# Performance work log

Hardware: AMD Instinct MI355X
Metric: run time of the kernel (lower is better)

The kernel has to match this reference:

```python
import jax, jax.numpy as jnp
import numpy as np

NUM_HEADS = 16


def setup_inputs() -> dict:
    key = jax.random.key(0)
    k1, k2, k3 = jax.random.split(key, 3)
    B, S, E = 2, 2048, 1024
    hidden_states = jax.random.normal(k1, (B, S, E), dtype=jnp.float32)
    c_attn_w = jax.random.normal(k2, (E, 3 * E), dtype=jnp.float32) * 0.02
    c_attn_b = jnp.zeros((3 * E,), dtype=jnp.float32)
    c_proj_w = jax.random.normal(k3, (E, E), dtype=jnp.float32) * 0.02
    c_proj_b = jnp.zeros((E,), dtype=jnp.float32)
    return {
        "hidden_states": hidden_states,
        "c_attn_w": c_attn_w,
        "c_attn_b": c_attn_b,
        "c_proj_w": c_proj_w,
        "c_proj_b": c_proj_b,
    }


def reference(hidden_states, c_attn_w, c_attn_b, c_proj_w, c_proj_b):
    B, S, E = hidden_states.shape
    H = NUM_HEADS
    D = E // H
    # Conv1D: qkv projection -> [B, S, 3E]
    qkv = jnp.einsum("bse,ef->bsf", hidden_states, c_attn_w) + c_attn_b
    q, k, v = jnp.split(qkv, 3, axis=-1)
    # split heads -> [B, H, S, D]
    def heads(x):
        return x.reshape(B, S, H, D).transpose(0, 2, 1, 3)
    q, k, v = heads(q), heads(k), heads(v)
    # scaled QK^T -> [B, H, S, S]
    scale = jnp.asarray(D, dtype=q.dtype) ** 0.5
    attn_weights = jnp.einsum("bhqd,bhkd->bhqk", q, k) / scale
    # causal mask (bias buffer): True on/below diagonal
    causal = jnp.tril(jnp.ones((S, S), dtype=bool))
    mask_value = jnp.finfo(attn_weights.dtype).min
    attn_weights = jnp.where(causal[None, None, :, :], attn_weights, mask_value)
    attn_weights = jax.nn.softmax(attn_weights, axis=-1)
    # attn @ V -> merge heads -> [B, S, E]
    attn_out = jnp.einsum("bhqk,bhkd->bhqd", attn_weights, v)
    attn_out = attn_out.transpose(0, 2, 1, 3).reshape(B, S, E)
    # output projection (Conv1D)
    out = jnp.einsum("bse,ef->bsf", attn_out, c_proj_w) + c_proj_b
    return out
```

## Files before the change

kernel.cpp:

```cpp
#include <hip/hip_runtime.h>
#include <stdint.h>

typedef __attribute__((ext_vector_type(8))) __bf16 bf16x8;
typedef __attribute__((ext_vector_type(4))) __bf16 bf16x4;
typedef __attribute__((ext_vector_type(4))) float f32x4;

#define MFMA16(a, b, c) __builtin_amdgcn_mfma_f32_16x16x32_bf16(a, b, c, 0, 0, 0)

__device__ __forceinline__ void async_ld16(const __bf16* g, __bf16* lds_base) {
    __builtin_amdgcn_global_load_lds(
        (const __attribute__((address_space(1))) void*)g,
        (__attribute__((address_space(3))) void*)lds_base, 16, 0, 0);
}

__global__ __launch_bounds__(256) void k_prep(
    const float* __restrict__ hs, const float* __restrict__ w1,
    const float* __restrict__ w2, __bf16* __restrict__ hsb,
    __bf16* __restrict__ w1t, __bf16* __restrict__ w2t) {
    __shared__ __bf16 tile[32][33];
    int bid = blockIdx.x, tid = threadIdx.x;
    if (bid < 4096) {
        int i = (bid * 256 + tid) * 4;
        float4 v = *(const float4*)(hs + i);
        bf16x4 o;
        o.x = (__bf16)v.x; o.y = (__bf16)v.y; o.z = (__bf16)v.z; o.w = (__bf16)v.w;
        *(bf16x4*)(hsb + i) = o;
        return;
    }
    const float* in; __bf16* out; int C, tb;
    if (bid < 7168) { in = w1; out = w1t; C = 3072; tb = bid - 4096; }
    else            { in = w2; out = w2t; C = 1024; tb = bid - 7168; }
    const int R = 1024;
    int ntc = C >> 5;
    int c0 = (tb % ntc) * 32, r0 = (tb / ntc) * 32;
    int tx = tid & 31, ty = tid >> 5;
#pragma unroll
    for (int i = 0; i < 4; i++)
        tile[ty + i * 8][tx] = (__bf16)in[(size_t)(r0 + ty + i * 8) * C + c0 + tx];
    __syncthreads();
#pragma unroll
    for (int i = 0; i < 4; i++)
        out[(size_t)(c0 + ty + i * 8) * R + r0 + tx] = tile[tx][ty + i * 8];
}

__global__ __launch_bounds__(256, 3) void k_gemm_qkv(
    const __bf16* __restrict__ A, const __bf16* __restrict__ Bt,
    const float* __restrict__ bias,
    __bf16* __restrict__ Qo, __bf16* __restrict__ Ko, __bf16* __restrict__ Vo) {
    __shared__ __bf16 As[128 * 64];
    __shared__ __bf16 Bs[128 * 64];
    const int Kd = 1024;
    int lid = blockIdx.x;
    int xcd = lid & 7, c = lid >> 3;
    int mi = (xcd >> 1) * 8 + c / 12;
    int ni = (xcd & 1) * 12 + c % 12;
    int n0 = ni * 128, m0 = mi * 128;
    bool tr = (ni < 16);
    int tid = threadIdx.x;
    int wv = tid >> 6, lane = tid & 63;
    int wm = (wv >> 1) * 64, wn = (wv & 1) * 64;
    int quad = lane >> 4, l16 = lane & 15;
    int rl = lane >> 3, sj = lane & 7;
    int sgo = (sj ^ rl) << 3;
    int swl = l16 & 7;
    const __bf16* p0 = tr ? Bs : As;
    const __bf16* p1 = tr ? As : Bs;
    int o0 = tr ? wn : wm, o1 = tr ? wm : wn;
    f32x4 acc[4][4] = {};
    for (int k0 = 0; k0 < Kd; k0 += 64) {
        __syncthreads();
#pragma unroll
        for (int r = 0; r < 4; r++) {
            int row = wv * 32 + r * 8;
            async_ld16(&A[(size_t)(m0 + row + rl) * Kd + k0 + sgo], &As[row * 64]);
            async_ld16(&Bt[(size_t)(n0 + row + rl) * Kd + k0 + sgo], &Bs[row * 64]);
        }
        __syncthreads();
#pragma unroll
        for (int ks = 0; ks < 2; ks++) {
            bf16x8 f0[4], f1[4];
#pragma unroll
            for (int i = 0; i < 4; i++)
                f0[i] = *(const bf16x8*)(
                    &p0[(o0 + i * 16 + l16) * 64 + (((ks * 4 + quad) ^ swl) << 3)]);
#pragma unroll
            for (int j = 0; j < 4; j++)
                f1[j] = *(const bf16x8*)(
                    &p1[(o1 + j * 16 + l16) * 64 + (((ks * 4 + quad) ^ swl) << 3)]);
#pragma unroll
            for (int i = 0; i < 4; i++)
#pragma unroll
                for (int j = 0; j < 4; j++)
                    acc[i][j] = MFMA16(f0[i], f1[j], acc[i][j]);
        }
    }
    if (tr) {
#pragma unroll
        for (int i = 0; i < 4; i++) {
#pragma unroll
            for (int j = 0; j < 4; j++) {
                int nb = n0 + wn + i * 16 + quad * 4;
                int sec = nb >> 10, nl = nb & 1023;
                int h = nl >> 6, d = nl & 63;
                int sg = m0 + wm + j * 16 + l16;
                int bb = sg >> 11, s = sg & 2047;
                f32x4 bv = *(const f32x4*)(&bias[nb]);
                __bf16* dst = (sec == 0) ? Qo : Ko;
                float scl = (sec == 0) ? 0.1803368801f : 1.0f;
                bf16x4 q4;
#pragma unroll
                for (int r = 0; r < 4; r++)
                    q4[r] = (__bf16)((acc[i][j][r] + bv[r]) * scl);
                *(bf16x4*)(&dst[((size_t)(bb * 16 + h) * 2048 + s) * 64 + d]) = q4;
            }
        }
    } else {
#pragma unroll
        for (int i = 0; i < 4; i++) {
#pragma unroll
            for (int j = 0; j < 4; j++) {
                int n = n0 + wn + j * 16 + l16;
                float bv = bias[n];
                int nl = n & 1023;
                int h = nl >> 6, d = nl & 63;
                int mbase = m0 + wm + i * 16 + quad * 4;
                int bb = mbase >> 11, s = mbase & 2047;
                bf16x4 v4;
#pragma unroll
                for (int r = 0; r < 4; r++) v4[r] = (__bf16)(acc[i][j][r] + bv);
                *(bf16x4*)(&Vo[((size_t)(bb * 16 + h) * 64 + d) * 2048 + s]) = v4;
            }
        }
    }
}

__global__ __launch_bounds__(256, 3) void k_gemm_proj(
    const __bf16* __restrict__ A, const __bf16* __restrict__ Bt,
    const float* __restrict__ bias, float* __restrict__ out) {
    __shared__ __bf16 As[64 * 64];
    __shared__ __bf16 Bs[128 * 64];
    const int Kd = 1024;
    int lid = blockIdx.x;
    int xcd = lid & 7, c = lid >> 3;
    int mi = xcd * 8 + (c >> 3);
    int ni = c & 7;
    int n0 = ni * 128, m0 = mi * 64;
    int tid = threadIdx.x;
    int wv = tid >> 6, lane = tid & 63;
    int wm = (wv >> 1) * 32, wn = (wv & 1) * 64;
    int quad = lane >> 4, l16 = lane & 15;
    int rl = lane >> 3, sj = lane & 7;
    int sgo = (sj ^ rl) << 3;
    int swl = l16 & 7;
    f32x4 acc[4][2] = {};
    for (int k0 = 0; k0 < Kd; k0 += 64) {
        __syncthreads();
#pragma unroll
        for (int r = 0; r < 2; r++) {
            int row = wv * 16 + r * 8;
            async_ld16(&A[(size_t)(m0 + row + rl) * Kd + k0 + sgo], &As[row * 64]);
        }
#pragma unroll
        for (int r = 0; r < 4; r++) {
            int row = wv * 32 + r * 8;
            async_ld16(&Bt[(size_t)(n0 + row + rl) * Kd + k0 + sgo], &Bs[row * 64]);
        }
        __syncthreads();
#pragma unroll
        for (int ks = 0; ks < 2; ks++) {
            bf16x8 f0[4], f1[2];
#pragma unroll
            for (int i = 0; i < 4; i++)
                f0[i] = *(const bf16x8*)(
                    &Bs[(wn + i * 16 + l16) * 64 + (((ks * 4 + quad) ^ swl) << 3)]);
#pragma unroll
            for (int j = 0; j < 2; j++)
                f1[j] = *(const bf16x8*)(
                    &As[(wm + j * 16 + l16) * 64 + (((ks * 4 + quad) ^ swl) << 3)]);
#pragma unroll
            for (int i = 0; i < 4; i++)
#pragma unroll
                for (int j = 0; j < 2; j++)
                    acc[i][j] = MFMA16(f0[i], f1[j], acc[i][j]);
        }
    }
#pragma unroll
    for (int i = 0; i < 4; i++) {
#pragma unroll
        for (int j = 0; j < 2; j++) {
            int nb = n0 + wn + i * 16 + quad * 4;
            int m = m0 + wm + j * 16 + l16;
            f32x4 bv = *(const f32x4*)(&bias[nb]);
            f32x4 o = acc[i][j] + bv;
            *(f32x4*)(&out[(size_t)m * 1024 + nb]) = o;
        }
    }
}

__device__ const int ATT_ORDER[24] = {7, 8, 10, 12, 14, 16, 18, 20, 22, 23, 6, 21,
                                      5, 19, 4, 17, 3, 15, 2, 13, 1, 11, 0, 9};

__global__ __launch_bounds__(256, 3) void k_attn(
    const __bf16* __restrict__ Qg, const __bf16* __restrict__ Kg,
    const __bf16* __restrict__ Vtg, __bf16* __restrict__ Op, float* __restrict__ Lp,
    __bf16* __restrict__ AOb) {
    __shared__ __bf16 Ksb[2][64 * 64];
    __shared__ __bf16 Vtb[2][64 * 64];
    __shared__ __bf16 Ps[128 * 72];
    int bh = blockIdx.x & 31;
    int slot = ATT_ORDER[blockIdx.x >> 5];
    int t, k0, k1;
    if (slot < 8) { t = slot; k0 = 0; k1 = 2 * t + 2; }
    else { int i2 = slot - 8; t = 8 + (i2 >> 1); k0 = (i2 & 1) * 16; k1 = min(k0 + 16, 2 * t + 2); }
    const __bf16* Qp = Qg + (size_t)bh * 2048 * 64;
    const __bf16* Kp = Kg + (size_t)bh * 2048 * 64;
    const __bf16* Vp = Vtg + (size_t)bh * 64 * 2048;
    int tid = threadIdx.x, wv = tid >> 6, lane = tid & 63;
    int quad = lane >> 4, l16 = lane & 15;
    int rl = lane >> 3, sj = lane & 7;
    int sgo = (sj ^ rl) << 3;
    int swl = l16 & 7;

    bf16x8 qf[2][2];
#pragma unroll
    for (int qn = 0; qn < 2; qn++)
#pragma unroll
        for (int ks = 0; ks < 2; ks++)
            qf[qn][ks] = *(const bf16x8*)(
                &Qp[(size_t)(t * 128 + wv * 32 + qn * 16 + l16) * 64 + ks * 32 + quad * 8]);
    const f32x4 zf = {0.f, 0.f, 0.f, 0.f};
    const __bf16 one1 = (__bf16)1.0f;
    const bf16x8 onesv = {one1, one1, one1, one1, one1, one1, one1, one1};
    f32x4 acc_l[2] = {zf, zf};
    f32x4 acc_o[2][4] = {};
    int qwmax = t * 128 + wv * 32 + 31;

    auto stage = [&](int buf, int kt) {
#pragma unroll
        for (int half = 0; half < 2; half++) {
            int r0 = wv * 16 + half * 8;
            async_ld16(&Kp[(size_t)(kt * 64 + r0 + rl) * 64 + sgo], &Ksb[buf][r0 * 64]);
            async_ld16(&Vp[(size_t)(r0 + rl) * 2048 + kt * 64 + sgo], &Vtb[buf][r0 * 64]);
        }
    };

    stage(0, k0);
    __syncthreads();

    for (int kt = k0; kt < k1; kt++) {
        int cur = (kt - k0) & 1;
        if (kt + 1 < k1) stage(cur ^ 1, kt + 1);
        if (kt * 64 <= qwmax) {
            const __bf16* Kc = Ksb[cur];
            const __bf16* Vc = Vtb[cur];
            f32x4 s[2][4];
#pragma unroll
            for (int ks = 0; ks < 2; ks++) {
                bf16x8 kf[4];
#pragma unroll
                for (int i = 0; i < 4; i++)
                    kf[i] = *(const bf16x8*)(
                        &Kc[(i * 16 + l16) * 64 + (((ks * 4 + quad) ^ swl) << 3)]);
                __builtin_amdgcn_s_setprio(1);
#pragma unroll
                for (int i = 0; i < 4; i++)
#pragma unroll
                    for (int qn = 0; qn < 2; qn++)
                        s[qn][i] = MFMA16(kf[i], qf[qn][ks], ks == 0 ? zf : s[qn][i]);
                __builtin_amdgcn_s_setprio(0);
            }
#pragma unroll
            for (int qn = 0; qn < 2; qn++) {
                int qmin = t * 128 + wv * 32 + qn * 16;
                if (kt * 64 + 63 > qmin) {
#pragma unroll
                    for (int i = 0; i < 4; i++)
#pragma unroll
                        for (int r = 0; r < 4; r++)
                            if (kt * 64 + i * 16 + quad * 4 + r > qmin + l16) s[qn][i][r] = -1e30f;
                }
            }
#pragma unroll
            for (int qn = 0; qn < 2; qn++)
#pragma unroll
                for (int i = 0; i < 4; i++) {
                    bf16x4 pk;
#pragma unroll
                    for (int r = 0; r < 4; r++) pk[r] = (__bf16)exp2f(s[qn][i][r]);
                    *(bf16x4*)(&Ps[(wv * 32 + qn * 16 + l16) * 72 + i * 16 + quad * 4]) = pk;
                }
#pragma unroll
            for (int ks = 0; ks < 2; ks++) {
                bf16x8 pf[2];
#pragma unroll
                for (int qn = 0; qn < 2; qn++)
                    pf[qn] = *(const bf16x8*)(
                        &Ps[(wv * 32 + qn * 16 + l16) * 72 + ks * 32 + quad * 8]);
                bf16x8 vf[4];
#pragma unroll
                for (int i = 0; i < 4; i++)
                    vf[i] = *(const bf16x8*)(
                        &Vc[(i * 16 + l16) * 64 + (((ks * 4 + quad) ^ swl) << 3)]);
                __builtin_amdgcn_s_setprio(1);
#pragma unroll
                for (int i = 0; i < 4; i++)
#pragma unroll
                    for (int qn = 0; qn < 2; qn++)
                        acc_o[qn][i] = MFMA16(vf[i], pf[qn], acc_o[qn][i]);
#pragma unroll
                for (int qn = 0; qn < 2; qn++)
                    acc_l[qn] = MFMA16(onesv, pf[qn], acc_l[qn]);
                __builtin_amdgcn_s_setprio(0);
            }
        }
        __syncthreads();
    }
    if (slot < 8) {
        int b = bh >> 4, h = bh & 15;
#pragma unroll
        for (int qn = 0; qn < 2; qn++) {
            float inv = 1.f / acc_l[qn][0];
            int q = t * 128 + wv * 32 + qn * 16 + l16;
#pragma unroll
            for (int i = 0; i < 4; i++) {
                bf16x4 o4;
#pragma unroll
                for (int r = 0; r < 4; r++) o4[r] = (__bf16)(acc_o[qn][i][r] * inv);
                *(bf16x4*)(&AOb[((size_t)b * 2048 + q) * 1024 + h * 64 +
                                i * 16 + quad * 4]) = o4;
            }
        }
    } else {
        size_t pbase = (size_t)slot * 32 + bh;
#pragma unroll
        for (int qn = 0; qn < 2; qn++) {
            float ls = acc_l[qn][0];
            int ql = wv * 32 + qn * 16 + l16;
            if (quad == 0) Lp[pbase * 128 + ql] = ls;
#pragma unroll
            for (int i = 0; i < 4; i++) {
                bf16x4 o4;
#pragma unroll
                for (int r = 0; r < 4; r++) o4[r] = (__bf16)acc_o[qn][i][r];
                *(bf16x4*)(&Op[(pbase * 128 + ql) * 64 + i * 16 + quad * 4]) = o4;
            }
        }
    }
}

__global__ __launch_bounds__(256) void k_attn_combine(
    const __bf16* __restrict__ Op, const float* __restrict__ Lp,
    __bf16* __restrict__ AOb) {
    int gid = blockIdx.x * 256 + threadIdx.x;
    int d4 = gid & 15;
    int q = 1024 + ((gid >> 4) & 1023);
    int bh = gid >> 14;
    int t = q >> 7, ql = q & 127;
    int base = 8 + 2 * (t - 8);
    float L = 0.f, o[4] = {};
#pragma unroll
    for (int c = 0; c < 2; c++) {
        size_t idx = (size_t)(base + c) * 32 + bh;
        L += Lp[idx * 128 + ql];
        bf16x4 p4 = *(const bf16x4*)(&Op[(idx * 128 + ql) * 64 + d4 * 4]);
#pragma unroll
        for (int r = 0; r < 4; r++) o[r] += (float)p4[r];
    }
    float inv = 1.f / L;
    int b = bh >> 4, h = bh & 15;
    bf16x4 o4;
#pragma unroll
    for (int r = 0; r < 4; r++) o4[r] = (__bf16)(o[r] * inv);
    *(bf16x4*)(&AOb[((size_t)b * 2048 + q) * 1024 + h * 64 + d4 * 4]) = o4;
}

extern "C" void kernel_launch(void* const* d_in, const int* in_sizes, int n_in,
                              void* d_out, int out_size, void* d_ws, size_t ws_size,
                              hipStream_t stream) {
    const float* hs = (const float*)d_in[0];
    const float* w1 = (const float*)d_in[1];
    const float* b1 = (const float*)d_in[2];
    const float* w2 = (const float*)d_in[3];
    const float* b2 = (const float*)d_in[4];
    float* out = (float*)d_out;

    char* ws = (char*)d_ws;
    __bf16* hsb = (__bf16*)(ws);
    __bf16* w1t = (__bf16*)(ws + (size_t)8 * 1024 * 1024);
    __bf16* w2t = (__bf16*)(ws + (size_t)14 * 1024 * 1024);
    __bf16* Qb  = (__bf16*)(ws + (size_t)16 * 1024 * 1024);
    __bf16* Kb  = (__bf16*)(ws + (size_t)24 * 1024 * 1024);
    __bf16* Vb  = (__bf16*)(ws + (size_t)32 * 1024 * 1024);
    __bf16* AOb = (__bf16*)(ws + (size_t)40 * 1024 * 1024);
    __bf16* Opart = (__bf16*)(ws);
    float*  Lpart = (float*)(ws + (size_t)13 * 1024 * 1024);

    k_prep<<<8192, 256, 0, stream>>>(hs, w1, w2, hsb, w1t, w2t);
    k_gemm_qkv<<<768, 256, 0, stream>>>(hsb, w1t, b1, Qb, Kb, Vb);
    k_attn<<<768, 256, 0, stream>>>(Qb, Kb, Vb, Opart, Lpart, AOb);
    k_attn_combine<<<2048, 256, 0, stream>>>(Opart, Lpart, AOb);
    k_gemm_proj<<<512, 256, 0, stream>>>(AOb, w2t, b2, out);
}
```

Before: 171.7 us.

## Double-buffer QKV GEMM LDS tiles with K-step 32 and prefetch

Restructures the QKV projection GEMM main loop to use two LDS buffers with a K tile of 32 instead of 64. The next tile's async global-to-LDS load is issued before the current tile's MFMAs, and each iteration needs one barrier instead of two. The XOR swizzle is removed in favour of a plain 32-wide row layout. This risks LDS bank conflicts on the fragment reads and doubles the loop trip count. It is also unclear whether the async load is guaranteed to complete before the barrier without an explicit vmcnt wait.

```diff
diff --git a/kernel.cpp b/kernel.cpp
--- a/kernel.cpp
+++ b/kernel.cpp
@@ -47,8 +47,8 @@
     const __bf16* __restrict__ A, const __bf16* __restrict__ Bt,
     const float* __restrict__ bias,
     __bf16* __restrict__ Qo, __bf16* __restrict__ Ko, __bf16* __restrict__ Vo) {
-    __shared__ __bf16 As[128 * 64];
-    __shared__ __bf16 Bs[128 * 64];
+    __shared__ __bf16 As[2][128 * 32];
+    __shared__ __bf16 Bs[2][128 * 32];
     const int Kd = 1024;
     int lid = blockIdx.x;
     int xcd = lid & 7, c = lid >> 3;
@@ -60,39 +60,40 @@
     int wv = tid >> 6, lane = tid & 63;
     int wm = (wv >> 1) * 64, wn = (wv & 1) * 64;
     int quad = lane >> 4, l16 = lane & 15;
-    int rl = lane >> 3, sj = lane & 7;
-    int sgo = (sj ^ rl) << 3;
-    int swl = l16 & 7;
-    const __bf16* p0 = tr ? Bs : As;
-    const __bf16* p1 = tr ? As : Bs;
+    int lrow = lane >> 2, lcol = (lane & 3) * 8;
     int o0 = tr ? wn : wm, o1 = tr ? wm : wn;
     f32x4 acc[4][4] = {};
-    for (int k0 = 0; k0 < Kd; k0 += 64) {
+
+    auto stage = [&](int buf, int k0) {
+#pragma unroll
+        for (int r = 0; r < 2; r++) {
+            int row = r * 64 + wv * 16;
+            async_ld16(&A[(size_t)(m0 + row + lrow) * Kd + k0 + lcol], &As[buf][row * 32]);
+            async_ld16(&Bt[(size_t)(n0 + row + lrow) * Kd + k0 + lcol], &Bs[buf][row * 32]);
+        }
+    };
+
+    stage(0, 0);
+    __syncthreads();
+
+    for (int kk = 0; kk < 32; kk++) {
+        int cur = kk & 1;
+        if (kk + 1 < 32) stage(cur ^ 1, (kk + 1) * 32);
+        const __bf16* p0 = tr ? Bs[cur] : As[cur];
+        const __bf16* p1 = tr ? As[cur] : Bs[cur];
+        bf16x8 f0[4], f1[4];
+#pragma unroll
+        for (int i = 0; i < 4; i++)
+            f0[i] = *(const bf16x8*)(&p0[(o0 + i * 16 + l16) * 32 + quad * 8]);
+#pragma unroll
+        for (int j = 0; j < 4; j++)
+            f1[j] = *(const bf16x8*)(&p1[(o1 + j * 16 + l16) * 32 + quad * 8]);
+#pragma unroll
+        for (int i = 0; i < 4; i++)
+#pragma unroll
+            for (int j = 0; j < 4; j++)
+                acc[i][j] = MFMA16(f0[i], f1[j], acc[i][j]);
         __syncthreads();
-#pragma unroll
-        for (int r = 0; r < 4; r++) {
-            int row = wv * 32 + r * 8;
-            async_ld16(&A[(size_t)(m0 + row + rl) * Kd + k0 + sgo], &As[row * 64]);
-            async_ld16(&Bt[(size_t)(n0 + row + rl) * Kd + k0 + sgo], &Bs[row * 64]);
-        }
-        __syncthreads();
-#pragma unroll
-        for (int ks = 0; ks < 2; ks++) {
-            bf16x8 f0[4], f1[4];
-#pragma unroll
-            for (int i = 0; i < 4; i++)
-                f0[i] = *(const bf16x8*)(
-                    &p0[(o0 + i * 16 + l16) * 64 + (((ks * 4 + quad) ^ swl) << 3)]);
-#pragma unroll
-            for (int j = 0; j < 4; j++)
-                f1[j] = *(const bf16x8*)(
-                    &p1[(o1 + j * 16 + l16) * 64 + (((ks * 4 + quad) ^ swl) << 3)]);
-#pragma unroll
-            for (int i = 0; i < 4; i++)
-#pragma unroll
-                for (int j = 0; j < 4; j++)
-                    acc[i][j] = MFMA16(f0[i], f1[j], acc[i][j]);
-        }
     }
     if (tr) {
 #pragma unroll
```

New measurement: 177.6 us. 1.03x slower.
